# Performance work log

Measured on AMD Instinct MI355X. Metric: run time of the kernel, lower is better.

Reference implementation:

```python
import jax, jax.numpy as jnp
import numpy as np
import math

N_GENES_TOTAL = 5000   # full gene table (fragments.n_genes)
N_CELLS_TOTAL = 10000  # full cell count (libsize buffer)
NBINS = 128            # spline components per gene
N_LATENT = 64
B = 256                # n_cells in minibatch
G = 2000               # genes_oi
NCUTS = 500_000


def setup_inputs() -> dict:
    key = jax.random.key(0)
    ks = jax.random.split(key, 12)
    latent = jax.random.normal(ks[0], (B, N_LATENT), jnp.float32)
    genes_oi = jax.random.randint(ks[1], (G,), 0, N_GENES_TOTAL)
    cells_oi = jax.random.randint(ks[2], (B,), 0, N_CELLS_TOTAL)
    cut_coordinates = jax.random.uniform(ks[3], (NCUTS,), jnp.float32)
    cut_local_cellxgene_ix = jax.random.randint(ks[4], (NCUTS,), 0, B * G)
    cut_local_gene_ix = jax.random.randint(ks[5], (NCUTS,), 0, G)
    local_cellxgene_ix = jax.random.randint(ks[6], (NCUTS,), 0, B * G)
    s = 1.0 / math.sqrt(N_LATENT)
    logit_weight = jax.random.uniform(ks[7], (N_GENES_TOTAL, N_LATENT, NBINS), jnp.float32, -s, s)
    rho_weight = jax.random.uniform(ks[8], (N_GENES_TOTAL, N_LATENT), jnp.float32, -s / 100.0, s / 100.0)
    rho_bias = jax.random.uniform(ks[9], (N_GENES_TOTAL,), jnp.float32, 1e-4, 1e-2)
    libsize = jax.random.randint(ks[10], (N_CELLS_TOTAL,), 1000, 20000)
    spline_heights = 0.01 * jax.random.normal(ks[11], (N_GENES_TOTAL, NBINS), jnp.float32)
    return {
        "latent": latent, "genes_oi": genes_oi, "cells_oi": cells_oi,
        "cut_coordinates": cut_coordinates,
        "cut_local_cellxgene_ix": cut_local_cellxgene_ix,
        "cut_local_gene_ix": cut_local_gene_ix,
        "local_cellxgene_ix": local_cellxgene_ix,
        "logit_weight": logit_weight, "rho_weight": rho_weight,
        "rho_bias": rho_bias, "libsize": libsize,
        "spline_heights": spline_heights,
        "n_cells": B, "n_genes": G,
    }


def reference(latent, genes_oi, cells_oi, cut_coordinates,
              cut_local_cellxgene_ix, cut_local_gene_ix, local_cellxgene_ix,
              logit_weight, rho_weight, rho_bias, libsize, spline_heights,
              n_cells, n_genes):
    # Decoder with n_layers=0: nn is identity
    lw = logit_weight[genes_oi]                     # [G, L, C]
    rw = rho_weight[genes_oi]                       # [G, L]
    mixture_delta = jnp.einsum('bl,glc->bgc', latent, lw)   # [B, G, C]
    rho_delta = latent @ rw.T                       # [B, G]

    # gather per-cut mixture deltas
    delta_flat = mixture_delta.reshape(n_cells * n_genes, -1)
    delta_cut = delta_flat[cut_local_cellxgene_ix]  # [Ncuts, C]

    # spline/mixture log-likelihood: per-gene histogram density with delta
    gene_heights = spline_heights[genes_oi]         # [G, C]
    h = gene_heights[cut_local_gene_ix] + delta_cut  # [Ncuts, C]
    logp_bins = jax.nn.log_softmax(h, axis=-1)
    nbins = h.shape[-1]
    bin_ix = jnp.clip((cut_coordinates * nbins).astype(jnp.int32), 0, nbins - 1)
    likelihood_mixture = (
        jnp.take_along_axis(logp_bins, bin_ix[:, None], axis=-1)[:, 0]
        + jnp.log(jnp.float32(nbins))
    )

    # Poisson fragment-count likelihood
    rate = (rho_bias[genes_oi][None, :] * jnp.exp(rho_delta)
            * libsize[cells_oi].astype(jnp.float32)[:, None])   # [B, G]
    counts = jnp.bincount(local_cellxgene_ix, length=n_cells * n_genes)
    counts = counts.reshape(n_cells, n_genes).astype(jnp.float32)
    ll_counts = counts * jnp.log(rate) - rate - jax.scipy.special.gammaln(counts + 1.0)

    likelihood = likelihood_mixture.sum() + ll_counts.sum()
    return -likelihood
```

## Files before the change

kernel.cpp:

```cpp
#include <hip/hip_runtime.h>

#define LDIM 64
#define CDIM 128
#define NREP 8
#define SUBCAP 64
#define MAXPER (NREP * SUBCAP)
#define LOG128 4.8520302639196171f

typedef __attribute__((ext_vector_type(8))) short bfrag;
typedef __attribute__((ext_vector_type(4))) float f32x4;

static __device__ __forceinline__ unsigned short f2bf(float f) {
    unsigned int x = __float_as_uint(f);
    unsigned int r = (x + 0x7fffu + ((x >> 16) & 1u)) >> 16;
    return (unsigned short)r;
}
static __device__ __forceinline__ float bf2f(unsigned int u) {
    return __uint_as_float(u << 16);
}

__global__ __launch_bounds__(256) void zero_kernel(uint4* __restrict__ p, size_t n16,
                                                   float* __restrict__ out, int out_size) {
    size_t i = (size_t)blockIdx.x * blockDim.x + threadIdx.x;
    size_t stride = (size_t)gridDim.x * blockDim.x;
    for (; i < n16; i += stride) p[i] = make_uint4(0u, 0u, 0u, 0u);
    if (blockIdx.x == 0 && threadIdx.x < (unsigned)out_size) out[threadIdx.x] = 0.f;
}

__global__ __launch_bounds__(256) void prep1_kernel(
    const float* __restrict__ heights, unsigned short* __restrict__ hbf, int nheights,
    const float* __restrict__ latent, unsigned short* __restrict__ latbf, int nlat,
    const int* __restrict__ cut_pair, const int* __restrict__ cut_gene,
    const float* __restrict__ coord, const int* __restrict__ genes_oi,
    const int* __restrict__ local_cxg, unsigned int* __restrict__ cnt_rep,
    unsigned int* __restrict__ bucket, unsigned int* __restrict__ countsT,
    int ncuts, int B, int G, int N, unsigned int magicG) {
    int stride = gridDim.x * blockDim.x;
    int rep = blockIdx.x & (NREP - 1);
    for (int i = blockIdx.x * blockDim.x + threadIdx.x; i < N; i += stride) {
        if (i < nheights) hbf[i] = f2bf(heights[i]);
        if (i < nlat) latbf[i] = f2bf(latent[i]);
        if (i < ncuts) {
            unsigned int p = (unsigned int)cut_pair[i];
            unsigned int cell = __umulhi(p, magicG);
            unsigned int g = p - cell * (unsigned int)G;
            unsigned int gg = (unsigned int)genes_oi[cut_gene[i]];
            int bin = (int)(coord[i] * 128.0f);
            bin = min(max(bin, 0), 127);
            unsigned int slot = atomicAdd(&cnt_rep[rep * G + (int)g], 1u);
            if (slot < SUBCAP)
                bucket[g * MAXPER + rep * SUBCAP + slot] =
                    (cell << 24) | (gg << 7) | (unsigned int)bin;
            unsigned int q = (unsigned int)local_cxg[i];
            unsigned int cell2 = __umulhi(q, magicG);
            unsigned int g2 = q - cell2 * (unsigned int)G;
            atomicAdd(&countsT[(size_t)g2 * (unsigned int)B + cell2], 1u);
        }
    }
}

__global__ __launch_bounds__(512, 2) void fused_kernel(
    const float* __restrict__ latent, const unsigned short* __restrict__ latbf,
    const int* __restrict__ genes_oi, const float* __restrict__ logit_weight,
    const unsigned short* __restrict__ hbf, const unsigned int* __restrict__ bucket,
    const unsigned int* __restrict__ cnt_rep, const unsigned int* __restrict__ countsT,
    const int* __restrict__ cells_oi,
    const float* __restrict__ rho_weight, const float* __restrict__ rho_bias,
    const int* __restrict__ libsize, int B, int G, float* __restrict__ out) {
    __shared__ unsigned short dlds[256 * CDIM];
    __shared__ unsigned short blds[CDIM * LDIM];
    int t = threadIdx.x;
    int g = blockIdx.x;
    int gene = genes_oi[g];

    {
        int n = t & 127;
        int k0 = (t >> 7) * 16;
        const float* src = logit_weight + (size_t)gene * LDIM * CDIM;
        float v[16];
        #pragma unroll
        for (int j = 0; j < 16; ++j) v[j] = src[(size_t)(k0 + j) * CDIM + n];
        #pragma unroll
        for (int h = 0; h < 2; ++h) {
            union { unsigned short u[8]; uint4 q; } pk;
            #pragma unroll
            for (int j = 0; j < 8; ++j) pk.u[j] = f2bf(v[h * 8 + j]);
            int kk = k0 + h * 8;
            *(uint4*)(blds + n * LDIM + (kk ^ ((n & 7) * 8))) = pk.q;
        }
    }
    __syncthreads();

    int wv = t >> 6, ln = t & 63;
    int l15 = ln & 15, l4 = ln >> 4;
    f32x4 acc[2][8];
    #pragma unroll
    for (int m = 0; m < 2; ++m)
        #pragma unroll
        for (int n = 0; n < 8; ++n) acc[m][n] = (f32x4){0.f, 0.f, 0.f, 0.f};

    #pragma unroll
    for (int ks = 0; ks < 2; ++ks) {
        int kk = ks * 32 + l4 * 8;
        bfrag a0 = *(const bfrag*)(latbf + (wv * 32 + l15) * LDIM + kk);
        bfrag a1 = *(const bfrag*)(latbf + (wv * 32 + 16 + l15) * LDIM + kk);
        #pragma unroll
        for (int n = 0; n < 8; ++n) {
            int col = n * 16 + l15;
            bfrag b = *(const bfrag*)(blds + col * LDIM + (kk ^ ((col & 7) * 8)));
            acc[0][n] = __builtin_amdgcn_mfma_f32_16x16x32_bf16(a0, b, acc[0][n], 0, 0, 0);
            acc[1][n] = __builtin_amdgcn_mfma_f32_16x16x32_bf16(a1, b, acc[1][n], 0, 0, 0);
        }
    }
    #pragma unroll
    for (int m = 0; m < 2; ++m)
        #pragma unroll
        for (int n = 0; n < 8; ++n)
            #pragma unroll
            for (int r = 0; r < 4; ++r) {
                int row = wv * 32 + m * 16 + l4 * 4 + r;
                int col = n * 16 + l15;
                dlds[row * CDIM + (col ^ ((row & 7) * 8))] = f2bf(acc[m][n][r]);
            }
    __syncthreads();

    float accs = 0.f;
    {
        const unsigned int* bk = bucket + (size_t)g * MAXPER;
        int grp = t >> 4, sub = t & 15;
        #pragma unroll
        for (int r = 0; r < NREP; ++r) {
            unsigned int cr = cnt_rep[r * G + g];
            if (cr > SUBCAP) cr = SUBCAP;
            const unsigned int* bs = bk + r * SUBCAP;
            for (unsigned int i = (unsigned int)grp; i < cr; i += 32u) {
                unsigned int rc = bs[i];
                int row = (int)(rc >> 24);
                unsigned int gg = (rc >> 7) & 0x1FFFu;
                uint4 dv = *(const uint4*)(dlds + row * CDIM + ((sub * 8) ^ ((row & 7) * 8)));
                uint4 hv = *(const uint4*)(hbf + ((size_t)gg << 7) + sub * 8);
                float h0 = bf2f(hv.x & 0xffffu) + bf2f(dv.x & 0xffffu);
                float h1 = bf2f(hv.x >> 16)     + bf2f(dv.x >> 16);
                float h2 = bf2f(hv.y & 0xffffu) + bf2f(dv.y & 0xffffu);
                float h3 = bf2f(hv.y >> 16)     + bf2f(dv.y >> 16);
                float h4 = bf2f(hv.z & 0xffffu) + bf2f(dv.z & 0xffffu);
                float h5 = bf2f(hv.z >> 16)     + bf2f(dv.z >> 16);
                float h6 = bf2f(hv.w & 0xffffu) + bf2f(dv.w & 0xffffu);
                float h7 = bf2f(hv.w >> 16)     + bf2f(dv.w >> 16);
                float m = fmaxf(fmaxf(fmaxf(h0, h1), fmaxf(h2, h3)),
                                fmaxf(fmaxf(h4, h5), fmaxf(h6, h7)));
                #pragma unroll
                for (int o = 1; o < 16; o <<= 1) m = fmaxf(m, __shfl_xor(m, o));
                float s = __expf(h0 - m) + __expf(h1 - m) + __expf(h2 - m) + __expf(h3 - m)
                        + __expf(h4 - m) + __expf(h5 - m) + __expf(h6 - m) + __expf(h7 - m);
                #pragma unroll
                for (int o = 1; o < 16; o <<= 1) s += __shfl_xor(s, o);
                int bin = (int)(rc & 127u);
                int e = bin & 7;
                float sel = h0;
                sel = (e == 1) ? h1 : sel;
                sel = (e == 2) ? h2 : sel;
                sel = (e == 3) ? h3 : sel;
                sel = (e == 4) ? h4 : sel;
                sel = (e == 5) ? h5 : sel;
                sel = (e == 6) ? h6 : sel;
                sel = (e == 7) ? h7 : sel;
                float hsel = __shfl(sel, (ln & 48) | (bin >> 3));
                if (sub == 0) accs += hsel - (m + __logf(s)) + LOG128;
            }
        }
    }

    if (t < B) {
        const float4* la = (const float4*)(latent + (size_t)t * LDIM);
        const float4* rw = (const float4*)(rho_weight + (size_t)gene * LDIM);
        float d = 0.f;
        #pragma unroll
        for (int k = 0; k < LDIM / 4; ++k) {
            float4 a = la[k], w = rw[k];
            d += a.x * w.x + a.y * w.y + a.z * w.z + a.w * w.w;
        }
        float rb = rho_bias[gene];
        float lib = (float)libsize[cells_oi[t]];
        float lrate = __logf(rb) + d + __logf(lib);
        float rate = __expf(lrate);
        unsigned int c = countsT[(size_t)g * B + t];
        float lgam = 0.f;
        for (unsigned int k = 2; k <= c; ++k) lgam += __logf((float)k);
        accs += (float)c * lrate - rate - lgam;
    }

    #pragma unroll
    for (int o = 32; o; o >>= 1) accs += __shfl_xor(accs, o);
    __syncthreads();
    float* red = (float*)blds;
    if (ln == 0) red[wv] = accs;
    __syncthreads();
    if (t == 0) {
        float s = red[0] + red[1] + red[2] + red[3] + red[4] + red[5] + red[6] + red[7];
        atomicAdd(out, -s);
    }
}

extern "C" void kernel_launch(void* const* d_in, const int* in_sizes, int n_in,
                              void* d_out, int out_size, void* d_ws, size_t ws_size,
                              hipStream_t stream) {
    const float* latent         = (const float*)d_in[0];
    const int*   genes_oi       = (const int*)d_in[1];
    const int*   cells_oi       = (const int*)d_in[2];
    const float* cut_coord      = (const float*)d_in[3];
    const int*   cut_pair       = (const int*)d_in[4];
    const int*   cut_gene       = (const int*)d_in[5];
    const int*   local_cxg      = (const int*)d_in[6];
    const float* logit_weight   = (const float*)d_in[7];
    const float* rho_weight     = (const float*)d_in[8];
    const float* rho_bias       = (const float*)d_in[9];
    const int*   libsize        = (const int*)d_in[10];
    const float* spline_heights = (const float*)d_in[11];
    int G = in_sizes[1];
    int B = in_sizes[2];
    int ncuts = in_sizes[4];
    int nheights = in_sizes[11];
    int nlat = B * LDIM;
    unsigned int magicG = (unsigned int)((0x100000000ULL + (unsigned)G - 1) / (unsigned)G);

    char* ws = (char*)d_ws;
    size_t off = 0;
    unsigned int* countsT = (unsigned int*)(ws + off);
    off += ((size_t)B * G * 4 + 255) & ~(size_t)255;
    unsigned int* cnt_rep = (unsigned int*)(ws + off);
    off += ((size_t)G * NREP * 4 + 255) & ~(size_t)255;
    size_t zero_bytes = off;
    unsigned int* bucket = (unsigned int*)(ws + off);
    off += ((size_t)G * MAXPER * 4 + 255) & ~(size_t)255;
    unsigned short* hbf = (unsigned short*)(ws + off);
    off += ((size_t)nheights * 2 + 255) & ~(size_t)255;
    unsigned short* latbf = (unsigned short*)(ws + off);
    off += ((size_t)nlat * 2 + 255) & ~(size_t)255;

    float* out = (float*)d_out;
    zero_kernel<<<1024, 256, 0, stream>>>((uint4*)ws, zero_bytes / 16, out, out_size);

    int N = ncuts > nheights ? ncuts : nheights;
    prep1_kernel<<<2048, 256, 0, stream>>>(
        spline_heights, hbf, nheights, latent, latbf, nlat,
        cut_pair, cut_gene, cut_coord, genes_oi, local_cxg,
        cnt_rep, bucket, countsT, ncuts, B, G, N, magicG);
    fused_kernel<<<G, 512, 0, stream>>>(
        latent, latbf, genes_oi, logit_weight, hbf, bucket,
        cnt_rep, countsT, cells_oi,
        rho_weight, rho_bias, libsize, B, G, out);
}
```

Before: 135.2 us.

## Split each gene across two blocks by cell half, compact buckets in LDS

Launches two blocks per gene, each handling 128 cells, with cut buckets keyed by gene and cell half. Bucket entries are compacted into shared memory and processed by 8-lane groups covering 16 bins each. The softmax drops its max subtraction and the occupancy hint is raised. The per-gene weight tile is now loaded and converted twice, and skipping the max shift relies on small logit magnitudes.

```diff
diff --git a/kernel.cpp b/kernel.cpp
--- a/kernel.cpp
+++ b/kernel.cpp
@@ -3,7 +3,7 @@
 #define LDIM 64
 #define CDIM 128
 #define NREP 8
-#define SUBCAP 64
+#define SUBCAP 48
 #define MAXPER (NREP * SUBCAP)
 #define LOG128 4.8520302639196171f
 
@@ -37,6 +37,7 @@
     int ncuts, int B, int G, int N, unsigned int magicG) {
     int stride = gridDim.x * blockDim.x;
     int rep = blockIdx.x & (NREP - 1);
+    int nb = 2 * G;
     for (int i = blockIdx.x * blockDim.x + threadIdx.x; i < N; i += stride) {
         if (i < nheights) hbf[i] = f2bf(heights[i]);
         if (i < nlat) latbf[i] = f2bf(latent[i]);
@@ -47,9 +48,10 @@
             unsigned int gg = (unsigned int)genes_oi[cut_gene[i]];
             int bin = (int)(coord[i] * 128.0f);
             bin = min(max(bin, 0), 127);
-            unsigned int slot = atomicAdd(&cnt_rep[rep * G + (int)g], 1u);
+            unsigned int bidx = g * 2u + (cell >> 7);
+            unsigned int slot = atomicAdd(&cnt_rep[rep * nb + (int)bidx], 1u);
             if (slot < SUBCAP)
-                bucket[g * MAXPER + rep * SUBCAP + slot] =
+                bucket[(size_t)bidx * MAXPER + rep * SUBCAP + slot] =
                     (cell << 24) | (gg << 7) | (unsigned int)bin;
             unsigned int q = (unsigned int)local_cxg[i];
             unsigned int cell2 = __umulhi(q, magicG);
@@ -59,7 +61,7 @@
     }
 }
 
-__global__ __launch_bounds__(512, 2) void fused_kernel(
+__global__ __launch_bounds__(512, 6) void fused_kernel(
     const float* __restrict__ latent, const unsigned short* __restrict__ latbf,
     const int* __restrict__ genes_oi, const float* __restrict__ logit_weight,
     const unsigned short* __restrict__ hbf, const unsigned int* __restrict__ bucket,
@@ -67,11 +69,16 @@
     const int* __restrict__ cells_oi,
     const float* __restrict__ rho_weight, const float* __restrict__ rho_bias,
     const int* __restrict__ libsize, int B, int G, float* __restrict__ out) {
-    __shared__ unsigned short dlds[256 * CDIM];
+    __shared__ unsigned short dlds[128 * CDIM];
     __shared__ unsigned short blds[CDIM * LDIM];
+    __shared__ unsigned int clds[MAXPER];
+    __shared__ unsigned int csum[NREP + 1];
+    __shared__ float red[8];
     int t = threadIdx.x;
-    int g = blockIdx.x;
+    int bid = blockIdx.x;
+    int g = bid >> 1, half = bid & 1;
     int gene = genes_oi[g];
+    int nb = 2 * G;
 
     {
         int n = t & 127;
@@ -89,90 +96,112 @@
             *(uint4*)(blds + n * LDIM + (kk ^ ((n & 7) * 8))) = pk.q;
         }
     }
+    if (t < NREP) csum[t + 1] = min(cnt_rep[t * nb + bid], (unsigned)SUBCAP);
     __syncthreads();
 
     int wv = t >> 6, ln = t & 63;
     int l15 = ln & 15, l4 = ln >> 4;
-    f32x4 acc[2][8];
-    #pragma unroll
-    for (int m = 0; m < 2; ++m)
-        #pragma unroll
-        for (int n = 0; n < 8; ++n) acc[m][n] = (f32x4){0.f, 0.f, 0.f, 0.f};
-
+    f32x4 acc[8];
+    #pragma unroll
+    for (int n = 0; n < 8; ++n) acc[n] = (f32x4){0.f, 0.f, 0.f, 0.f};
     #pragma unroll
     for (int ks = 0; ks < 2; ++ks) {
         int kk = ks * 32 + l4 * 8;
-        bfrag a0 = *(const bfrag*)(latbf + (wv * 32 + l15) * LDIM + kk);
-        bfrag a1 = *(const bfrag*)(latbf + (wv * 32 + 16 + l15) * LDIM + kk);
+        bfrag a = *(const bfrag*)(latbf + (half * 128 + wv * 16 + l15) * LDIM + kk);
         #pragma unroll
         for (int n = 0; n < 8; ++n) {
             int col = n * 16 + l15;
             bfrag b = *(const bfrag*)(blds + col * LDIM + (kk ^ ((col & 7) * 8)));
-            acc[0][n] = __builtin_amdgcn_mfma_f32_16x16x32_bf16(a0, b, acc[0][n], 0, 0, 0);
-            acc[1][n] = __builtin_amdgcn_mfma_f32_16x16x32_bf16(a1, b, acc[1][n], 0, 0, 0);
-        }
-    }
-    #pragma unroll
-    for (int m = 0; m < 2; ++m)
-        #pragma unroll
-        for (int n = 0; n < 8; ++n)
-            #pragma unroll
-            for (int r = 0; r < 4; ++r) {
-                int row = wv * 32 + m * 16 + l4 * 4 + r;
-                int col = n * 16 + l15;
-                dlds[row * CDIM + (col ^ ((row & 7) * 8))] = f2bf(acc[m][n][r]);
-            }
+            acc[n] = __builtin_amdgcn_mfma_f32_16x16x32_bf16(a, b, acc[n], 0, 0, 0);
+        }
+    }
+    #pragma unroll
+    for (int n = 0; n < 8; ++n)
+        #pragma unroll
+        for (int r = 0; r < 4; ++r) {
+            int row = wv * 16 + l4 * 4 + r;
+            int col = n * 16 + l15;
+            dlds[row * CDIM + (col ^ ((row & 7) * 8))] = f2bf(acc[n][r]);
+        }
+    if (t == 0) {
+        csum[0] = 0;
+        #pragma unroll
+        for (int r = 0; r < NREP; ++r) csum[r + 1] += csum[r];
+    }
+    __syncthreads();
+
+    {
+        const unsigned int* bk = bucket + (size_t)bid * MAXPER;
+        #pragma unroll
+        for (int r = 0; r < NREP; ++r) {
+            unsigned int base = csum[r], cr = csum[r + 1] - base;
+            for (unsigned int i = (unsigned int)t; i < cr; i += 512u)
+                clds[base + i] = bk[r * SUBCAP + i];
+        }
+    }
     __syncthreads();
 
     float accs = 0.f;
     {
-        const unsigned int* bk = bucket + (size_t)g * MAXPER;
-        int grp = t >> 4, sub = t & 15;
-        #pragma unroll
-        for (int r = 0; r < NREP; ++r) {
-            unsigned int cr = cnt_rep[r * G + g];
-            if (cr > SUBCAP) cr = SUBCAP;
-            const unsigned int* bs = bk + r * SUBCAP;
-            for (unsigned int i = (unsigned int)grp; i < cr; i += 32u) {
-                unsigned int rc = bs[i];
-                int row = (int)(rc >> 24);
-                unsigned int gg = (rc >> 7) & 0x1FFFu;
-                uint4 dv = *(const uint4*)(dlds + row * CDIM + ((sub * 8) ^ ((row & 7) * 8)));
-                uint4 hv = *(const uint4*)(hbf + ((size_t)gg << 7) + sub * 8);
-                float h0 = bf2f(hv.x & 0xffffu) + bf2f(dv.x & 0xffffu);
-                float h1 = bf2f(hv.x >> 16)     + bf2f(dv.x >> 16);
-                float h2 = bf2f(hv.y & 0xffffu) + bf2f(dv.y & 0xffffu);
-                float h3 = bf2f(hv.y >> 16)     + bf2f(dv.y >> 16);
-                float h4 = bf2f(hv.z & 0xffffu) + bf2f(dv.z & 0xffffu);
-                float h5 = bf2f(hv.z >> 16)     + bf2f(dv.z >> 16);
-                float h6 = bf2f(hv.w & 0xffffu) + bf2f(dv.w & 0xffffu);
-                float h7 = bf2f(hv.w >> 16)     + bf2f(dv.w >> 16);
-                float m = fmaxf(fmaxf(fmaxf(h0, h1), fmaxf(h2, h3)),
-                                fmaxf(fmaxf(h4, h5), fmaxf(h6, h7)));
-                #pragma unroll
-                for (int o = 1; o < 16; o <<= 1) m = fmaxf(m, __shfl_xor(m, o));
-                float s = __expf(h0 - m) + __expf(h1 - m) + __expf(h2 - m) + __expf(h3 - m)
-                        + __expf(h4 - m) + __expf(h5 - m) + __expf(h6 - m) + __expf(h7 - m);
-                #pragma unroll
-                for (int o = 1; o < 16; o <<= 1) s += __shfl_xor(s, o);
-                int bin = (int)(rc & 127u);
-                int e = bin & 7;
-                float sel = h0;
-                sel = (e == 1) ? h1 : sel;
-                sel = (e == 2) ? h2 : sel;
-                sel = (e == 3) ? h3 : sel;
-                sel = (e == 4) ? h4 : sel;
-                sel = (e == 5) ? h5 : sel;
-                sel = (e == 6) ? h6 : sel;
-                sel = (e == 7) ? h7 : sel;
-                float hsel = __shfl(sel, (ln & 48) | (bin >> 3));
-                if (sub == 0) accs += hsel - (m + __logf(s)) + LOG128;
-            }
-        }
-    }
-
-    if (t < B) {
-        const float4* la = (const float4*)(latent + (size_t)t * LDIM);
+        unsigned int C = csum[NREP];
+        int grp = t >> 3, sub = t & 7;
+        for (unsigned int i = (unsigned int)grp; i < C; i += 64u) {
+            unsigned int rc = clds[i];
+            int row = (int)((rc >> 24) & 127u);
+            unsigned int gg = (rc >> 7) & 0x1FFFu;
+            int sw = (row & 7) * 8;
+            uint4 dva = *(const uint4*)(dlds + row * CDIM + ((sub * 16) ^ sw));
+            uint4 dvb = *(const uint4*)(dlds + row * CDIM + ((sub * 16 + 8) ^ sw));
+            const uint4* hp = (const uint4*)(hbf + ((size_t)gg << 7) + sub * 16);
+            uint4 hva = hp[0], hvb = hp[1];
+            float h0  = bf2f(hva.x & 0xffffu) + bf2f(dva.x & 0xffffu);
+            float h1  = bf2f(hva.x >> 16)     + bf2f(dva.x >> 16);
+            float h2  = bf2f(hva.y & 0xffffu) + bf2f(dva.y & 0xffffu);
+            float h3  = bf2f(hva.y >> 16)     + bf2f(dva.y >> 16);
+            float h4  = bf2f(hva.z & 0xffffu) + bf2f(dva.z & 0xffffu);
+            float h5  = bf2f(hva.z >> 16)     + bf2f(dva.z >> 16);
+            float h6  = bf2f(hva.w & 0xffffu) + bf2f(dva.w & 0xffffu);
+            float h7  = bf2f(hva.w >> 16)     + bf2f(dva.w >> 16);
+            float h8  = bf2f(hvb.x & 0xffffu) + bf2f(dvb.x & 0xffffu);
+            float h9  = bf2f(hvb.x >> 16)     + bf2f(dvb.x >> 16);
+            float h10 = bf2f(hvb.y & 0xffffu) + bf2f(dvb.y & 0xffffu);
+            float h11 = bf2f(hvb.y >> 16)     + bf2f(dvb.y >> 16);
+            float h12 = bf2f(hvb.z & 0xffffu) + bf2f(dvb.z & 0xffffu);
+            float h13 = bf2f(hvb.z >> 16)     + bf2f(dvb.z >> 16);
+            float h14 = bf2f(hvb.w & 0xffffu) + bf2f(dvb.w & 0xffffu);
+            float h15 = bf2f(hvb.w >> 16)     + bf2f(dvb.w >> 16);
+            float s = __expf(h0)  + __expf(h1)  + __expf(h2)  + __expf(h3)
+                    + __expf(h4)  + __expf(h5)  + __expf(h6)  + __expf(h7)
+                    + __expf(h8)  + __expf(h9)  + __expf(h10) + __expf(h11)
+                    + __expf(h12) + __expf(h13) + __expf(h14) + __expf(h15);
+            #pragma unroll
+            for (int o = 1; o < 8; o <<= 1) s += __shfl_xor(s, o);
+            int bin = (int)(rc & 127u);
+            int e = bin & 15;
+            float sel = h0;
+            sel = (e == 1)  ? h1  : sel;
+            sel = (e == 2)  ? h2  : sel;
+            sel = (e == 3)  ? h3  : sel;
+            sel = (e == 4)  ? h4  : sel;
+            sel = (e == 5)  ? h5  : sel;
+            sel = (e == 6)  ? h6  : sel;
+            sel = (e == 7)  ? h7  : sel;
+            sel = (e == 8)  ? h8  : sel;
+            sel = (e == 9)  ? h9  : sel;
+            sel = (e == 10) ? h10 : sel;
+            sel = (e == 11) ? h11 : sel;
+            sel = (e == 12) ? h12 : sel;
+            sel = (e == 13) ? h13 : sel;
+            sel = (e == 14) ? h14 : sel;
+            sel = (e == 15) ? h15 : sel;
+            float hsel = __shfl(sel, (ln & 56) | (bin >> 4));
+            if (sub == 0) accs += hsel - __logf(s) + LOG128;
+        }
+    }
+
+    if (t < 128) {
+        int cell = half * 128 + t;
+        const float4* la = (const float4*)(latent + (size_t)cell * LDIM);
         const float4* rw = (const float4*)(rho_weight + (size_t)gene * LDIM);
         float d = 0.f;
         #pragma unroll
@@ -181,10 +210,10 @@
             d += a.x * w.x + a.y * w.y + a.z * w.z + a.w * w.w;
         }
         float rb = rho_bias[gene];
-        float lib = (float)libsize[cells_oi[t]];
+        float lib = (float)libsize[cells_oi[cell]];
         float lrate = __logf(rb) + d + __logf(lib);
         float rate = __expf(lrate);
-        unsigned int c = countsT[(size_t)g * B + t];
+        unsigned int c = countsT[(size_t)g * B + cell];
         float lgam = 0.f;
         for (unsigned int k = 2; k <= c; ++k) lgam += __logf((float)k);
         accs += (float)c * lrate - rate - lgam;
@@ -192,8 +221,6 @@
 
     #pragma unroll
     for (int o = 32; o; o >>= 1) accs += __shfl_xor(accs, o);
-    __syncthreads();
-    float* red = (float*)blds;
     if (ln == 0) red[wv] = accs;
     __syncthreads();
     if (t == 0) {
@@ -229,10 +256,10 @@
     unsigned int* countsT = (unsigned int*)(ws + off);
     off += ((size_t)B * G * 4 + 255) & ~(size_t)255;
     unsigned int* cnt_rep = (unsigned int*)(ws + off);
-    off += ((size_t)G * NREP * 4 + 255) & ~(size_t)255;
+    off += ((size_t)2 * G * NREP * 4 + 255) & ~(size_t)255;
     size_t zero_bytes = off;
     unsigned int* bucket = (unsigned int*)(ws + off);
-    off += ((size_t)G * MAXPER * 4 + 255) & ~(size_t)255;
+    off += ((size_t)2 * G * MAXPER * 4 + 255) & ~(size_t)255;
     unsigned short* hbf = (unsigned short*)(ws + off);
     off += ((size_t)nheights * 2 + 255) & ~(size_t)255;
     unsigned short* latbf = (unsigned short*)(ws + off);
@@ -246,7 +273,7 @@
         spline_heights, hbf, nheights, latent, latbf, nlat,
         cut_pair, cut_gene, cut_coord, genes_oi, local_cxg,
         cnt_rep, bucket, countsT, ncuts, B, G, N, magicG);
-    fused_kernel<<<G, 512, 0, stream>>>(
+    fused_kernel<<<2 * G, 512, 0, stream>>>(
         latent, latbf, genes_oi, logit_weight, hbf, bucket,
         cnt_rep, countsT, cells_oi,
         rho_weight, rho_bias, libsize, B, G, out);
```

After: 139.3 us. 3.0% more time.
